# Kernel optimization log

Measured on AMD Instinct MI355X. Metric: run time of the kernel, lower is better.

## Reference

```python
import jax, jax.numpy as jnp
import numpy as np

N_P = 200000  # points (literals)
N_C = 50000   # constraints (clauses)
D = 64
VOCAB = 400   # max_size**2 = 20**2


def setup_inputs() -> dict:
    key = jax.random.key(0)
    ks = jax.random.split(key, 12)
    s = 0.05
    inp = {}
    inp["embedding"] = jax.random.normal(ks[0], (VOCAB, D)) * s
    inp["cls_bias"] = jnp.zeros((VOCAB,))
    inp["W_cinit"] = jax.random.normal(ks[1], (D, 1)) * s
    inp["b_cinit"] = jnp.zeros((D,))
    # clause LSTMs stacked in c_t order: 0=equi, 1=square, 2=diamond, 3=midpoint
    inp["Wih_c"] = jax.random.normal(ks[2], (4, 4 * D, 4 * D)) * s
    inp["Whh_c"] = jax.random.normal(ks[3], (4, 4 * D, D)) * s
    inp["bih_c"] = jnp.zeros((4, 4 * D))
    inp["bhh_c"] = jnp.zeros((4, 4 * D))
    # point-update LSTM L_u
    inp["Wih_u"] = jax.random.normal(ks[4], (4 * D, D)) * s
    inp["Whh_u"] = jax.random.normal(ks[5], (4 * D, D)) * s
    inp["bih_u"] = jnp.zeros((4 * D,))
    inp["bhh_u"] = jnp.zeros((4 * D,))
    inp["x_p_rand"] = jax.random.uniform(ks[6], (N_P, D))
    inp["y"] = jax.random.randint(ks[7], (N_P,), 0, VOCAB)
    inp["p_t"] = jax.random.randint(ks[8], (N_P,), 0, 2)
    inp["c_t"] = jax.random.randint(ks[9], (N_C,), 0, 4)
    inp["p2c"] = jax.random.randint(ks[10], (N_C, 4), 0, N_P)
    inp["num_iters"] = 2
    return inp


def _lstm_cell(x, h, c, Wih, Whh, bih, bhh):
    # torch nn.LSTM single-step cell, gate order (i, f, g, o)
    gates = x @ Wih.T + bih + h @ Whh.T + bhh
    i, f, g, o = jnp.split(gates, 4, axis=-1)
    c_new = jax.nn.sigmoid(f) * c + jax.nn.sigmoid(i) * jnp.tanh(g)
    h_new = jax.nn.sigmoid(o) * jnp.tanh(c_new)
    return h_new, c_new


def reference(embedding, cls_bias, W_cinit, b_cinit, Wih_c, Whh_c, bih_c, bhh_c,
              Wih_u, Whh_u, bih_u, bhh_u, x_p_rand, y, p_t, c_t, p2c, num_iters):
    n_p, d = x_p_rand.shape
    n_c = c_t.shape[0]
    fixed = (p_t != 0)[:, None]  # fixed points keep their embedding
    x_p = jnp.where(fixed, embedding[y], x_p_rand)
    c_init = W_cinit[:, 0] + b_cinit  # C_init(ones(1))
    x_c = jnp.broadcast_to(c_init, (n_c, d))
    x_p_h = jnp.zeros_like(x_p)
    x_c_h = jnp.zeros_like(x_c)
    sel = jax.nn.one_hot(c_t, 4, dtype=x_p.dtype)  # [n_c, 4] clause-type selector
    flat_p2c = p2c.reshape(-1)
    for _ in range(num_iters):
        # LC: gather the 4 points of each constraint
        vars_ = x_p[p2c]  # [n_c, 4, d]
        vars_full = vars_.reshape(n_c, 4 * d)
        vars_mid = vars_.at[:, 3].set(0.0).reshape(n_c, 4 * d)  # midpoint zeros 4th slot
        hs, cs = [], []
        for tp in range(4):
            inp_t = vars_mid if tp == 3 else vars_full
            h_t, c_new = _lstm_cell(inp_t, x_c, x_c_h, Wih_c[tp], Whh_c[tp], bih_c[tp], bhh_c[tp])
            hs.append(h_t)
            cs.append(c_new)
        hs = jnp.stack(hs)  # [4, n_c, d]
        cs = jnp.stack(cs)
        x_c = jnp.einsum('tnd,nt->nd', hs, sel)
        x_c_h = jnp.einsum('tnd,nt->nd', cs, sel)
        # CL: msg = adj.T @ x_c, i.e. scatter-add x_c over incidence edges
        msg = jax.ops.segment_sum(jnp.repeat(x_c, 4, axis=0), flat_p2c, num_segments=n_p)
        h_u, c_u = _lstm_cell(msg, x_p, x_p_h, Wih_u, Whh_u, bih_u, bhh_u)
        # only variable points are updated; fixed points keep old state
        x_p = jnp.where(fixed, x_p, h_u)
        x_p_h = jnp.where(fixed, x_p_h, c_u)
    logits = x_p @ embedding.T + cls_bias  # tied classifier
    return logits
```

## Files before the change

### kernel.cpp

```cpp
#include <hip/hip_runtime.h>
#include <hip/hip_bf16.h>

#define DD 64
#define GG 256
#define BK 16

typedef __attribute__((ext_vector_type(8))) __bf16 bfrag;
typedef __attribute__((ext_vector_type(4))) float f32x4;

__device__ __forceinline__ float sigmf(float x){ return 1.f/(1.f+__expf(-x)); }
__device__ __forceinline__ float tanhfast(float x){ return 1.f - 2.f/(__expf(2.f*x)+1.f); }
__device__ __forceinline__ short bf16c(float f){
  __hip_bfloat16 h = __float2bfloat16(f);
  return *reinterpret_cast<short*>(&h);
}

__global__ void k_setup(
    const float* __restrict__ Wihc, const float* __restrict__ Whhc,
    const float* __restrict__ Wihu, const float* __restrict__ Whhu,
    const float* __restrict__ emb, const float* __restrict__ Wci,
    const float* __restrict__ bci, const float* __restrict__ xpr,
    const int* __restrict__ y, const int* __restrict__ pt,
    const int* __restrict__ ct, const int* __restrict__ p2c,
    short* __restrict__ Wc_lay, short* __restrict__ Wu_lay,
    short* __restrict__ E_lay,
    short* __restrict__ xp_bf, short* __restrict__ xc_bf,
    int* __restrict__ tlist, int* __restrict__ cnt,
    int* __restrict__ vlist, int* __restrict__ cnt2,
    int* __restrict__ cursor, int* __restrict__ elist, int NP, int NC)
{
  int b = blockIdx.x;
  const int t = threadIdx.x;
  if (b < 1280){
    int idx = b*256 + t;
    int tp = idx / 81920, r = idx % 81920;
    int ks = r / 8192;  int r2 = r % 8192;
    int nt = r2 / 512;  int r3 = r2 % 512;
    int lr = r3 / 32;   int r4 = r3 % 32;
    int lk = r4 / 8,    e  = r4 % 8;
    int g = nt*16 + lr, k = ks*32 + lk*8 + e;
    float v = (k < 256) ? Wihc[((size_t)tp*256+g)*256 + k]
                        : Whhc[((size_t)tp*256+g)*64 + (k-256)];
    Wc_lay[idx] = bf16c(v);
    return;
  }
  b -= 1280;
  if (b < 128){
    int idx = b*256 + t;
    int ks = idx / 8192; int r2 = idx % 8192;
    int nt = r2 / 512;   int r3 = r2 % 512;
    int lr = r3 / 32;    int r4 = r3 % 32;
    int lk = r4 / 8,     e  = r4 % 8;
    int g = nt*16 + lr, k = ks*32 + lk*8 + e;
    float v = (k < 64) ? Wihu[g*64 + k] : Whhu[g*64 + (k-64)];
    Wu_lay[idx] = bf16c(v);
    return;
  }
  b -= 128;
  if (b < 100){
    int idx = b*256 + t;
    int ks = idx / 12800; int r = idx % 12800;
    int nt = r / 512;     int r3 = r % 512;
    int lr = r3 / 32;     int r4 = r3 % 32;
    int lk = r4 / 8,      e  = r4 % 8;
    int v = nt*16 + lr, k = ks*32 + lk*8 + e;
    E_lay[idx] = bf16c(emb[v*64 + k]);
    return;
  }
  b -= 100;
  int nbP4 = (NP*4 + 255) >> 8;
  if (b < nbP4){
    int i = b*256 + t;
    if (i < NP*4){
      int p = i >> 2, ch = i & 3;
      const float* src = (pt[p]!=0) ? (emb + (size_t)y[p]*DD + ch*16)
                                    : (xpr + (size_t)p*DD + ch*16);
      short o[16];
      #pragma unroll
      for (int f4=0; f4<4; ++f4){
        float4 v = ((const float4*)src)[f4];
        o[f4*4+0]=bf16c(v.x); o[f4*4+1]=bf16c(v.y); o[f4*4+2]=bf16c(v.z); o[f4*4+3]=bf16c(v.w);
      }
      *(uint4*)(xp_bf + (size_t)p*DD + ch*16)     = *(uint4*)&o[0];
      *(uint4*)(xp_bf + (size_t)p*DD + ch*16 + 8) = *(uint4*)&o[8];
    }
    return;
  }
  b -= nbP4;
  int nbC4 = (NC*4 + 255) >> 8;
  if (b < nbC4){
    int i = b*256 + t;
    if (i < NC*4){
      int c = i >> 2, ch = i & 3;
      short o[16];
      #pragma unroll
      for (int d=0; d<16; ++d) o[d] = bf16c(Wci[ch*16+d] + bci[ch*16+d]);
      *(uint4*)(xc_bf + (size_t)c*DD + ch*16)     = *(uint4*)&o[0];
      *(uint4*)(xc_bf + (size_t)c*DD + ch*16 + 8) = *(uint4*)&o[8];
    }
    return;
  }
  b -= nbC4;
  int nbCl = (NC + 255) >> 8;
  if (b < nbCl){
    int c = b*256 + t;
    int lane = t & 63;
    int tp = (c < NC) ? ct[c] : -1;
    unsigned long long lt = (lane == 63) ? ~0ull >> 1 : ((1ull << lane) - 1ull);
    #pragma unroll
    for (int ty=0; ty<4; ++ty){
      unsigned long long m = __ballot(tp==ty);
      if (m == 0ull) continue;
      int nw = __popcll(m), rank = __popcll(m & lt);
      int leader = __ffsll((long long)m) - 1;
      int base = 0;
      if (lane == leader) base = atomicAdd(cnt + ty, nw);
      base = __shfl(base, leader);
      if (tp == ty) tlist[ty*NC + base + rank] = c;
    }
    return;
  }
  b -= nbCl;
  int nbCp = (NP + 255) >> 8;
  if (b < nbCp){
    int p = b*256 + t;
    int lane = t & 63;
    bool var = (p < NP) && (pt[p]==0);
    unsigned long long lt = (lane == 63) ? ~0ull >> 1 : ((1ull << lane) - 1ull);
    unsigned long long m = __ballot(var);
    if (m){
      int nw = __popcll(m), rank = __popcll(m & lt);
      int leader = __ffsll((long long)m) - 1;
      int base = 0;
      if (lane == leader) base = atomicAdd(cnt2, nw);
      base = __shfl(base, leader);
      if (var) vlist[base + rank] = p;
    }
    return;
  }
  b -= nbCp;
  {
    int e = b*256 + t;
    if (e < NC*4){
      int p = p2c[e];
      int pos = atomicAdd(cursor + p, 1);
      if (pos < BK) elist[p*BK + pos] = e >> 2;
    }
  }
}

__launch_bounds__(256)
__global__ void k_clause(const short* __restrict__ Wc_lay,
                         const float* __restrict__ bih, const float* __restrict__ bhh,
                         const short* __restrict__ xp_bf,
                         short* __restrict__ xc_bf, float* __restrict__ xch,
                         const int* __restrict__ p2c, const int* __restrict__ tlist,
                         const int* __restrict__ cnt, int NC, int first){
  __shared__ __align__(16) short As[64][264];
  int tp, n, base;
  {
    const int c0=cnt[0], c1=cnt[1], c2=cnt[2], c3=cnt[3];
    int b = blockIdx.x;
    const int t0=(c0+63)>>6;
    if (b < t0){ tp=0; n=c0; base=b<<6; }
    else { b-=t0; const int t1=(c1+63)>>6;
      if (b < t1){ tp=1; n=c1; base=b<<6; }
      else { b-=t1; const int t2=(c2+63)>>6;
        if (b < t2){ tp=2; n=c2; base=b<<6; }
        else { b-=t2; const int t3=(c3+63)>>6;
          if (b < t3){ tp=3; n=c3; base=b<<6; } else return; } } }
  }
  const int t = threadIdx.x;
  {
    int row = t >> 2, ch = t & 3;
    int idx = base + row;
    int c = (idx < n) ? tlist[tp*NC + idx] : -1;
    #pragma unroll
    for (int slot=0; slot<4; ++slot){
      uint4 v0 = make_uint4(0,0,0,0), v1 = make_uint4(0,0,0,0);
      if (c >= 0 && !(tp==3 && slot==3)){
        int p = p2c[c*4 + slot];
        const short* src = xp_bf + (size_t)p*DD + ch*16;
        v0 = *(const uint4*)src; v1 = *(const uint4*)(src+8);
      }
      *(uint4*)&As[row][slot*64 + ch*16 + 0] = v0;
      *(uint4*)&As[row][slot*64 + ch*16 + 8] = v1;
    }
  }
  const int lane = t & 63, w = t >> 6;
  const int lr = lane & 15, lk = lane >> 4;
  const int arow = base + w*16 + lr;
  const int ac = (arow < n) ? tlist[tp*NC + arow] : -1;
  const bfrag ZERO = (bfrag){0,0,0,0,0,0,0,0};
  __syncthreads();
  f32x4 acc[16];
  #pragma unroll
  for (int i=0;i<16;i++) acc[i] = (f32x4){0.f,0.f,0.f,0.f};
  const short* wb = Wc_lay + (size_t)tp*81920 + (lr*4 + lk)*8;
  #pragma unroll
  for (int ks=0; ks<10; ++ks){
    bfrag a;
    if (ks < 8) a = *(const bfrag*)&As[w*16 + lr][ks*32 + lk*8];
    else        a = (ac >= 0) ? *(const bfrag*)(xc_bf + (size_t)ac*DD + (ks-8)*32 + lk*8) : ZERO;
    #pragma unroll
    for (int nt=0; nt<16; ++nt){
      bfrag bv = *(const bfrag*)(wb + (ks*16 + nt)*512);
      acc[nt] = __builtin_amdgcn_mfma_f32_16x16x32_bf16(a, bv, acc[nt], 0, 0, 0);
    }
  }
  #pragma unroll
  for (int r=0; r<4; ++r){
    int idx = base + w*16 + lk*4 + r;
    if (idx >= n) continue;
    int c = tlist[tp*NC + idx];
    #pragma unroll
    for (int q=0; q<4; ++q){
      int d = lr + 16*q;
      float gi = acc[q][r]    + bih[tp*GG + d]       + bhh[tp*GG + d];
      float gf = acc[4+q][r]  + bih[tp*GG + 64 + d]  + bhh[tp*GG + 64 + d];
      float gn = acc[8+q][r]  + bih[tp*GG + 128 + d] + bhh[tp*GG + 128 + d];
      float go = acc[12+q][r] + bih[tp*GG + 192 + d] + bhh[tp*GG + 192 + d];
      float cold = first ? 0.f : xch[(size_t)c*DD + d];
      float cn = sigmf(gf)*cold + sigmf(gi)*tanhfast(gn);
      float hn = sigmf(go)*tanhfast(cn);
      xc_bf[(size_t)c*DD + d] = bf16c(hn);
      xch[(size_t)c*DD + d]   = cn;
    }
  }
}

__launch_bounds__(256)
__global__ void k_point(const short* __restrict__ Wu_lay,
                        const float* __restrict__ bihu, const float* __restrict__ bhhu,
                        const short* __restrict__ xc_bf,
                        const int* __restrict__ cursor, const int* __restrict__ elist,
                        const int* __restrict__ vlist, const int* __restrict__ nvp,
                        short* __restrict__ xp_bf, float* __restrict__ xph,
                        int NP, int first){
  const int nv = nvp[0];
  const int base = blockIdx.x*64;
  if (base >= nv) return;
  __shared__ __align__(16) short As[64][136];
  const int t = threadIdx.x;
  {
    int row = t >> 2, ch = t & 3;
    int idx = base + row;
    int gr = (idx < nv) ? vlist[idx] : -1;
    float s[16];
    #pragma unroll
    for (int z=0; z<16; ++z) s[z] = 0.f;
    uint4 xv0 = make_uint4(0,0,0,0), xv1 = make_uint4(0,0,0,0);
    if (gr >= 0){
      int dg = cursor[gr]; if (dg > BK) dg = BK;
      for (int j=0; j<dg; ++j){
        int c = elist[gr*BK + j];
        const uint4* xcp = (const uint4*)(xc_bf + (size_t)c*DD + ch*16);
        uint4 u0 = xcp[0], u1 = xcp[1];
        uint ua[8] = {u0.x,u0.y,u0.z,u0.w,u1.x,u1.y,u1.z,u1.w};
        #pragma unroll
        for (int i2=0;i2<8;i2++){
          s[i2*2]   += __uint_as_float(ua[i2] << 16);
          s[i2*2+1] += __uint_as_float(ua[i2] & 0xffff0000u);
        }
      }
      const uint4* xpp = (const uint4*)(xp_bf + (size_t)gr*DD + ch*16);
      xv0 = xpp[0]; xv1 = xpp[1];
    }
    short os[16];
    #pragma unroll
    for (int z=0; z<16; ++z) os[z] = bf16c(s[z]);
    *(uint4*)&As[row][ch*16 + 0] = *(uint4*)&os[0];
    *(uint4*)&As[row][ch*16 + 8] = *(uint4*)&os[8];
    *(uint4*)&As[row][64 + ch*16 + 0] = xv0;
    *(uint4*)&As[row][64 + ch*16 + 8] = xv1;
  }
  __syncthreads();
  const int lane = t & 63, w = t >> 6;
  const int lr = lane & 15, lk = lane >> 4;
  f32x4 acc[16];
  #pragma unroll
  for (int i=0;i<16;i++) acc[i] = (f32x4){0.f,0.f,0.f,0.f};
  const short* wb = Wu_lay + (lr*4 + lk)*8;
  #pragma unroll
  for (int ks=0; ks<4; ++ks){
    bfrag a = *(const bfrag*)&As[w*16 + lr][ks*32 + lk*8];
    #pragma unroll
    for (int nt=0; nt<16; ++nt){
      bfrag bv = *(const bfrag*)(wb + (ks*16 + nt)*512);
      acc[nt] = __builtin_amdgcn_mfma_f32_16x16x32_bf16(a, bv, acc[nt], 0, 0, 0);
    }
  }
  #pragma unroll
  for (int r=0; r<4; ++r){
    int idx = base + w*16 + lk*4 + r;
    if (idx >= nv) continue;
    int m = vlist[idx];
    #pragma unroll
    for (int q=0; q<4; ++q){
      int d = lr + 16*q;
      float gi = acc[q][r]    + bihu[d]       + bhhu[d];
      float gf = acc[4+q][r]  + bihu[64 + d]  + bhhu[64 + d];
      float gn = acc[8+q][r]  + bihu[128 + d] + bhhu[128 + d];
      float go = acc[12+q][r] + bihu[192 + d] + bhhu[192 + d];
      float cold = first ? 0.f : xph[(size_t)idx*DD + d];
      float cn = sigmf(gf)*cold + sigmf(gi)*tanhfast(gn);
      float hn = sigmf(go)*tanhfast(cn);
      xp_bf[(size_t)m*DD + d] = bf16c(hn);
      xph[(size_t)idx*DD + d] = cn;
    }
  }
}

#define ST 212
__launch_bounds__(256)
__global__ void k_logits(const short* __restrict__ xp_bf, const short* __restrict__ E_lay,
                         const float* __restrict__ cbias,
                         float* __restrict__ out, int NP, int V){
  const int base = blockIdx.x*64;
  __shared__ __align__(16) char smem[64*ST*4];
  short (*As)[72] = (short (*)[72])smem;
  float (*T)[ST]  = (float (*)[ST])smem;
  const int t = threadIdx.x;
  {
    int row = t >> 2, ch = t & 3;
    int gr = base + row;
    uint4 v0 = make_uint4(0,0,0,0), v1 = make_uint4(0,0,0,0);
    if (gr < NP){
      const uint4* src = (const uint4*)(xp_bf + (size_t)gr*DD + ch*16);
      v0 = src[0]; v1 = src[1];
    }
    *(uint4*)&As[row][ch*16 + 0] = v0;
    *(uint4*)&As[row][ch*16 + 8] = v1;
  }
  __syncthreads();
  const int lane = t & 63, w = t >> 6;
  const int lr = lane & 15, lk = lane >> 4;
  f32x4 acc[25];
  #pragma unroll
  for (int i=0;i<25;i++) acc[i] = (f32x4){0.f,0.f,0.f,0.f};
  const short* wb = E_lay + (lr*4 + lk)*8;
  #pragma unroll
  for (int ks=0; ks<2; ++ks){
    bfrag a = *(const bfrag*)&As[w*16 + lr][ks*32 + lk*8];
    #pragma unroll
    for (int nt=0; nt<25; ++nt){
      bfrag bv = *(const bfrag*)(wb + (ks*25 + nt)*512);
      acc[nt] = __builtin_amdgcn_mfma_f32_16x16x32_bf16(a, bv, acc[nt], 0, 0, 0);
    }
  }
  #pragma unroll
  for (int chunk=0; chunk<2; ++chunk){
    const int nt0 = chunk ? 13 : 0;
    const int nt1 = chunk ? 25 : 13;
    const int cb  = nt0*16;
    const int nc4 = chunk ? 48 : 52;
    __syncthreads();
    #pragma unroll
    for (int nt=nt0; nt<nt1; ++nt){
      float cbv = cbias[nt*16 + lr];
      #pragma unroll
      for (int r=0; r<4; ++r)
        T[w*16 + lk*4 + r][nt*16 + lr - cb] = acc[nt][r] + cbv;
    }
    __syncthreads();
    #pragma unroll
    for (int rr=0; rr<16; ++rr){
      int row = w*16 + rr;
      int m = base + row;
      if (m < NP && lane < nc4){
        f32x4 vv = *(f32x4*)&T[row][lane*4];
        __builtin_nontemporal_store(vv, (f32x4*)(out + (size_t)m*V + cb + lane*4));
      }
    }
  }
}

extern "C" void kernel_launch(void* const* d_in, const int* in_sizes, int n_in,
                              void* d_out, int out_size, void* d_ws, size_t ws_size,
                              hipStream_t stream){
  const float* emb   = (const float*)d_in[0];
  const float* cbias = (const float*)d_in[1];
  const float* Wci   = (const float*)d_in[2];
  const float* bci   = (const float*)d_in[3];
  const float* Wihc  = (const float*)d_in[4];
  const float* Whhc  = (const float*)d_in[5];
  const float* bihc  = (const float*)d_in[6];
  const float* bhhc  = (const float*)d_in[7];
  const float* Wihu  = (const float*)d_in[8];
  const float* Whhu  = (const float*)d_in[9];
  const float* bihu  = (const float*)d_in[10];
  const float* bhhu  = (const float*)d_in[11];
  const float* xpr   = (const float*)d_in[12];
  const int* y    = (const int*)d_in[13];
  const int* pt   = (const int*)d_in[14];
  const int* ct   = (const int*)d_in[15];
  const int* p2c  = (const int*)d_in[16];
  const int NP = in_sizes[13];
  const int NC = in_sizes[15];
  const int V  = in_sizes[1];
  const int NE = NC*4;

  char* w = (char*)d_ws;
  auto alloc = [&](size_t bytes)->char*{ char* p = w; w += (bytes + 255) & ~255ull; return p; };
  short* xp_bf = (short*)alloc((size_t)NP*DD*2);
  float* xph   = (float*)alloc((size_t)NP*DD*4);
  short* xc_bf = (short*)alloc((size_t)NC*DD*2);
  float* xch   = (float*)alloc((size_t)NC*DD*4);
  int*   tlist = (int*)alloc((size_t)4*NC*4);
  short* Wc_lay= (short*)alloc((size_t)327680*2);
  short* Wu_lay= (short*)alloc((size_t)32768*2);
  short* E_lay = (short*)alloc((size_t)25600*2);
  int*   cursor  = (int*)alloc((size_t)NP*4);
  int*   ctr     = (int*)alloc(256);
  int*   elist   = (int*)alloc((size_t)NP*BK*4);
  int*   vlist   = (int*)alloc((size_t)NP*4);
  int* cnt  = ctr;
  int* cnt2 = ctr + 16;

  const int NB   = (NP + 255)/256;
  const int nbP4 = (NP*4 + 255)/256;
  const int nbC4 = (NC*4 + 255)/256;
  const int nbCl = (NC + 255)/256;
  const int nbCp = NB;
  const int nbE  = (NE + 255)/256;
  const int g_setup = 1280 + 128 + 100 + nbP4 + nbC4 + nbCl + nbCp + nbE;

  hipMemsetAsync(cursor, 0, (size_t)NP*4 + 256, stream);
  k_setup<<<g_setup, 256, 0, stream>>>(Wihc, Whhc, Wihu, Whhu, emb, Wci, bci, xpr,
                                       y, pt, ct, p2c,
                                       Wc_lay, Wu_lay, E_lay,
                                       xp_bf, xc_bf,
                                       tlist, cnt, vlist, cnt2, cursor, elist, NP, NC);

  const int ctiles = (NC+63)/64 + 3;
  const int ptiles = (NP+63)/64;
  const int num_iters = 2;
  for (int it=0; it<num_iters; ++it){
    k_clause<<<ctiles, 256, 0, stream>>>(Wc_lay, bihc, bhhc, xp_bf, xc_bf, xch,
                                         p2c, tlist, cnt, NC, it==0);
    k_point<<<ptiles, 256, 0, stream>>>(Wu_lay, bihu, bhhu, xc_bf,
                                        cursor, elist, vlist, cnt2,
                                        xp_bf, xph, NP, it==0);
  }
  k_logits<<<(NP+63)/64, 256, 0, stream>>>(xp_bf, E_lay, cbias, (float*)d_out, NP, V);
}
```

Baseline: 381.9 us.

## Transpose logits MFMA so each lane owns a point row and stores directly

The logits kernel swaps the MFMA operand roles: embedding fragments become the A operand and point features the B operand, so each lane's accumulator holds four consecutive vocab entries for one point. Results are written straight from registers as 16-byte stores, which removes the shared-memory staging, the LDS transpose and all block barriers. Accumulators are split into two halves of 13 and 12 tiles to reduce register pressure. The cost is that each lane writes 16 bytes to a different row, so stores are less coalesced than the earlier row-contiguous pattern.

```diff
diff --git a/kernel.cpp b/kernel.cpp
--- a/kernel.cpp
+++ b/kernel.cpp
@@ -311,65 +311,64 @@
   }
 }
 
-#define ST 212
 __launch_bounds__(256)
 __global__ void k_logits(const short* __restrict__ xp_bf, const short* __restrict__ E_lay,
                          const float* __restrict__ cbias,
                          float* __restrict__ out, int NP, int V){
-  const int base = blockIdx.x*64;
-  __shared__ __align__(16) char smem[64*ST*4];
-  short (*As)[72] = (short (*)[72])smem;
-  float (*T)[ST]  = (float (*)[ST])smem;
   const int t = threadIdx.x;
-  {
-    int row = t >> 2, ch = t & 3;
-    int gr = base + row;
-    uint4 v0 = make_uint4(0,0,0,0), v1 = make_uint4(0,0,0,0);
-    if (gr < NP){
-      const uint4* src = (const uint4*)(xp_bf + (size_t)gr*DD + ch*16);
-      v0 = src[0]; v1 = src[1];
-    }
-    *(uint4*)&As[row][ch*16 + 0] = v0;
-    *(uint4*)&As[row][ch*16 + 8] = v1;
-  }
-  __syncthreads();
   const int lane = t & 63, w = t >> 6;
   const int lr = lane & 15, lk = lane >> 4;
-  f32x4 acc[25];
-  #pragma unroll
-  for (int i=0;i<25;i++) acc[i] = (f32x4){0.f,0.f,0.f,0.f};
-  const short* wb = E_lay + (lr*4 + lk)*8;
-  #pragma unroll
-  for (int ks=0; ks<2; ++ks){
-    bfrag a = *(const bfrag*)&As[w*16 + lr][ks*32 + lk*8];
-    #pragma unroll
-    for (int nt=0; nt<25; ++nt){
-      bfrag bv = *(const bfrag*)(wb + (ks*25 + nt)*512);
-      acc[nt] = __builtin_amdgcn_mfma_f32_16x16x32_bf16(a, bv, acc[nt], 0, 0, 0);
-    }
-  }
-  #pragma unroll
-  for (int chunk=0; chunk<2; ++chunk){
-    const int nt0 = chunk ? 13 : 0;
-    const int nt1 = chunk ? 25 : 13;
-    const int cb  = nt0*16;
-    const int nc4 = chunk ? 48 : 52;
-    __syncthreads();
-    #pragma unroll
-    for (int nt=nt0; nt<nt1; ++nt){
-      float cbv = cbias[nt*16 + lr];
+  const int p = blockIdx.x*64 + w*16 + lr;
+  const bool ok = p < NP;
+  bfrag b0, b1;
+  if (ok){
+    b0 = *(const bfrag*)(xp_bf + (size_t)p*DD + lk*8);
+    b1 = *(const bfrag*)(xp_bf + (size_t)p*DD + 32 + lk*8);
+  } else { b0 = (bfrag){0,0,0,0,0,0,0,0}; b1 = b0; }
+  const short* ab = E_lay + (lr*4 + lk)*8;
+  {
+    f32x4 acc[13];
+    #pragma unroll
+    for (int j=0;j<13;j++) acc[j] = (f32x4){0.f,0.f,0.f,0.f};
+    #pragma unroll
+    for (int j=0;j<13;j++){
+      bfrag a0 = *(const bfrag*)(ab + j*512);
+      acc[j] = __builtin_amdgcn_mfma_f32_16x16x32_bf16(a0, b0, acc[j], 0, 0, 0);
+      bfrag a1 = *(const bfrag*)(ab + (25 + j)*512);
+      acc[j] = __builtin_amdgcn_mfma_f32_16x16x32_bf16(a1, b1, acc[j], 0, 0, 0);
+    }
+    if (ok){
       #pragma unroll
-      for (int r=0; r<4; ++r)
-        T[w*16 + lk*4 + r][nt*16 + lr - cb] = acc[nt][r] + cbv;
-    }
-    __syncthreads();
-    #pragma unroll
-    for (int rr=0; rr<16; ++rr){
-      int row = w*16 + rr;
-      int m = base + row;
-      if (m < NP && lane < nc4){
-        f32x4 vv = *(f32x4*)&T[row][lane*4];
-        __builtin_nontemporal_store(vv, (f32x4*)(out + (size_t)m*V + cb + lane*4));
+      for (int j=0;j<13;j++){
+        int v = j*16 + lk*4;
+        float4 cb = *(const float4*)(cbias + v);
+        f32x4 r;
+        r[0] = acc[j][0] + cb.x; r[1] = acc[j][1] + cb.y;
+        r[2] = acc[j][2] + cb.z; r[3] = acc[j][3] + cb.w;
+        __builtin_nontemporal_store(r, (f32x4*)(out + (size_t)p*V + v));
+      }
+    }
+  }
+  {
+    f32x4 acc[12];
+    #pragma unroll
+    for (int j=0;j<12;j++) acc[j] = (f32x4){0.f,0.f,0.f,0.f};
+    #pragma unroll
+    for (int j=0;j<12;j++){
+      bfrag a0 = *(const bfrag*)(ab + (13 + j)*512);
+      acc[j] = __builtin_amdgcn_mfma_f32_16x16x32_bf16(a0, b0, acc[j], 0, 0, 0);
+      bfrag a1 = *(const bfrag*)(ab + (25 + 13 + j)*512);
+      acc[j] = __builtin_amdgcn_mfma_f32_16x16x32_bf16(a1, b1, acc[j], 0, 0, 0);
+    }
+    if (ok){
+      #pragma unroll
+      for (int j=0;j<12;j++){
+        int v = (13 + j)*16 + lk*4;
+        float4 cb = *(const float4*)(cbias + v);
+        f32x4 r;
+        r[0] = acc[j][0] + cb.x; r[1] = acc[j][1] + cb.y;
+        r[2] = acc[j][2] + cb.z; r[3] = acc[j][3] + cb.w;
+        __builtin_nontemporal_store(r, (f32x4*)(out + (size_t)p*V + v));
       }
     }
   }
```

After: 418.2 us. 1.1x slower.
